# Performance work log

Measured on AMD Instinct MI355X. Metric: run time of the kernel, lower is better.

The kernel has to match this reference:

```python
import jax, jax.numpy as jnp
import numpy as np

BS, C, H, W, KSZ, NH = 4, 64, 64, 64, 7, 8
CH = 8 * C  # positional FFN hidden width (channels*8)


def _extract_nbhd(x, k):
    """x: (bs,h,w,d) -> (bs, h*w, k*k, d). Zero-padded k x k neighborhoods
    (the torch module unfolds the *projected* features, so padding zeros are
    zero keys/values, exactly as here)."""
    bs, h, w, d = x.shape
    p = k - 1
    xp = jnp.pad(x, ((0, 0), (p // 2, p - p // 2), (p // 2, p - p // 2), (0, 0)))
    shifts = [xp[:, di:di + h, dj:dj + w, :] for di in range(k) for dj in range(k)]
    patches = jnp.stack(shifts, axis=3)  # (bs, h, w, r, d)
    return patches.reshape(bs, h * w, k * k, d)


def setup_inputs() -> dict:
    key = jax.random.key(0)
    ks = jax.random.split(key, 8)

    def lin_w(kk, fan_in, fan_out):
        s = 1.0 / np.sqrt(fan_in)
        return jax.random.uniform(kk, (fan_in, fan_out), jnp.float32, -s, s)

    return {
        "x": jax.random.normal(ks[0], (BS, C, H, W), jnp.float32),
        "WQ_w": lin_w(ks[1], C, C), "WQ_b": jnp.zeros((C,), jnp.float32),
        "WK_w": lin_w(ks[2], C, C), "WK_b": jnp.zeros((C,), jnp.float32),
        "WV_w": lin_w(ks[3], C, C), "WV_b": jnp.zeros((C,), jnp.float32),
        "WO_w": lin_w(ks[4], C, C), "WO_b": jnp.zeros((C,), jnp.float32),
        "pos_w1": lin_w(ks[5], 2, CH), "pos_b1": jnp.zeros((CH,), jnp.float32),
        "pos_w2": lin_w(ks[6], CH, NH), "pos_b2": jnp.zeros((NH,), jnp.float32),
    }


def reference(x, WQ_w, WQ_b, WK_w, WK_b, WV_w, WV_b, WO_w, WO_b,
              pos_w1, pos_b1, pos_w2, pos_b2):
    bs, c, h, w = x.shape
    n, r, nh = h * w, KSZ * KSZ, NH
    dh = c // nh

    # ---- positional bias: FFN on relative coordinates of each k x k window ----
    gi, gj = jnp.meshgrid(jnp.linspace(-3.0, 3.0, h), jnp.linspace(-3.0, 3.0, w),
                          indexing='ij')
    coords = jnp.stack([gi, gj], axis=-1)                 # (h, w, 2)
    nb_coords = _extract_nbhd(coords[None], KSZ)          # (1, n, r, 2)
    rel = nb_coords - coords.reshape(1, n, 1, 2)          # (1, n, r, 2)
    P = jax.nn.relu(rel @ pos_w1 + pos_b1) @ pos_w2 + pos_b2   # (1, n, r, nh)

    # ---- restricted multi-head self attention over k x k neighborhoods ----
    xi = x.transpose(0, 2, 3, 1)                          # (bs, h, w, c)
    Q = (xi.reshape(bs, n, c) @ WQ_w + WQ_b).reshape(bs, n, nh, dh)
    Kn = _extract_nbhd(xi @ WK_w + WK_b, KSZ).reshape(bs, n, r, nh, dh)
    Vn = _extract_nbhd(xi @ WV_w + WV_b, KSZ).reshape(bs, n, r, nh, dh)

    scores = jnp.einsum('bnhd,bnrhd->bnhr', Q, Kn) / np.sqrt(dh).astype(np.float32)
    scores = scores + P.transpose(0, 1, 3, 2)             # bias per head, broadcast bs
    wts = jax.nn.softmax(scores, axis=-1)                 # (bs, n, nh, r)
    o = jnp.einsum('bnhr,bnrhd->bnhd', wts, Vn).reshape(bs, n, c)
    o = o @ WO_w + WO_b
    return o.reshape(bs, h, w, c).transpose(0, 3, 1, 2)   # (bs, c, h, w)
```

## Files before the change

kernel.cpp:

```cpp
#include <hip/hip_runtime.h>
#include <hip/hip_bf16.h>
#include <math.h>

#define NPIX   4096
#define STEPF  (6.0f/63.0f)
#define SCALE  0.35355339059327373f

#define OFF_PT 0
#define OFF_PB 4096
#define OFF_Q  65536
#define OFF_K  (OFF_Q + 1048576)
#define OFF_V  (OFF_K + 1048576)
#define OFF_O  (OFF_V + 1048576)

__global__ __launch_bounds__(256) void pos_ffn_kernel(
    const float* __restrict__ w1, const float* __restrict__ b1,
    const float* __restrict__ w2, const float* __restrict__ b2,
    float* __restrict__ PT, float* __restrict__ PB)
{
    __shared__ float s_w1[1024];
    __shared__ float s_b1[512];
    __shared__ float s_w2[4096];
    int tid = threadIdx.x;
    for (int idx = tid; idx < 5632; idx += 256) {
        if (idx < 1024)       s_w1[idx]        = w1[idx];
        else if (idx < 1536)  s_b1[idx - 1024] = b1[idx - 1024];
        else                  s_w2[idx - 1536] = w2[idx - 1536];
    }
    __syncthreads();

    int gid = blockIdx.x * 256 + tid;
    int e  = gid >> 3;
    int lg = gid & 7;
    if (e >= 49 + NPIX) return;

    float r0, r1;
    if (e < 49) {
        int di = e / 7, dj = e % 7;
        r0 = (float)(di - 3) * STEPF;
        r1 = (float)(dj - 3) * STEPF;
    } else {
        int p = e - 49;
        r0 = 3.0f - (float)(p >> 6) * STEPF;
        r1 = 3.0f - (float)(p & 63) * STEPF;
    }

    float acc[8] = {0.f,0.f,0.f,0.f,0.f,0.f,0.f,0.f};
    #pragma unroll 8
    for (int kk = 0; kk < 64; ++kk) {
        int k = (kk << 3) + lg;
        float hv = fmaf(r0, s_w1[k], fmaf(r1, s_w1[512 + k], s_b1[k]));
        hv = fmaxf(hv, 0.0f);
        const float4 wa = *(const float4*)&s_w2[k * 8];
        const float4 wb = *(const float4*)&s_w2[k * 8 + 4];
        acc[0] = fmaf(hv, wa.x, acc[0]);
        acc[1] = fmaf(hv, wa.y, acc[1]);
        acc[2] = fmaf(hv, wa.z, acc[2]);
        acc[3] = fmaf(hv, wa.w, acc[3]);
        acc[4] = fmaf(hv, wb.x, acc[4]);
        acc[5] = fmaf(hv, wb.y, acc[5]);
        acc[6] = fmaf(hv, wb.z, acc[6]);
        acc[7] = fmaf(hv, wb.w, acc[7]);
    }
    #pragma unroll
    for (int m = 1; m < 8; m <<= 1) {
        #pragma unroll
        for (int j = 0; j < 8; ++j) acc[j] += __shfl_xor(acc[j], m);
    }
    float v = acc[lg] + b2[lg];
    if (e < 49) PT[e * 8 + lg] = v;
    else        PB[(e - 49) * 8 + lg] = v;
}

__global__ __launch_bounds__(256) void qkv_kernel(
    const float* __restrict__ x,
    const float* __restrict__ wq, const float* __restrict__ bq,
    const float* __restrict__ wk, const float* __restrict__ bk,
    const float* __restrict__ wv, const float* __restrict__ bv,
    float* __restrict__ Qo, float* __restrict__ Ko, float* __restrict__ Vo)
{
    __shared__ float s_W[4096];
    __shared__ float s_b[64];
    const float* W; const float* bias; float* out;
    if (blockIdx.y == 0)      { W = wq; bias = bq; out = Qo; }
    else if (blockIdx.y == 1) { W = wk; bias = bk; out = Ko; }
    else                      { W = wv; bias = bv; out = Vo; }

    int tid = threadIdx.x;
    {
        const float4* W4 = (const float4*)W;
        float4* s4 = (float4*)s_W;
        #pragma unroll
        for (int q = 0; q < 4; ++q) s4[tid + q * 256] = W4[tid + q * 256];
    }
    if (tid < 64) s_b[tid] = bias[tid];
    __syncthreads();

    int jg = tid & 3;
    int pl = tid >> 2;
    int g  = blockIdx.x * 64 + pl;
    int b  = g >> 12;
    int p  = g & 4095;
    const float* xb = x + ((size_t)b << 18) + p;

    float acc[16];
    #pragma unroll
    for (int j = 0; j < 16; ++j) acc[j] = s_b[(jg << 4) + j];

    #pragma unroll 8
    for (int c = 0; c < 64; ++c) {
        float xv = xb[(size_t)c << 12];
        const float* wr = &s_W[(c << 6) + (jg << 4)];
        const float4 w0 = *(const float4*)(wr + 0);
        const float4 w1v = *(const float4*)(wr + 4);
        const float4 w2v = *(const float4*)(wr + 8);
        const float4 w3v = *(const float4*)(wr + 12);
        acc[0]  = fmaf(xv, w0.x,  acc[0]);  acc[1]  = fmaf(xv, w0.y,  acc[1]);
        acc[2]  = fmaf(xv, w0.z,  acc[2]);  acc[3]  = fmaf(xv, w0.w,  acc[3]);
        acc[4]  = fmaf(xv, w1v.x, acc[4]);  acc[5]  = fmaf(xv, w1v.y, acc[5]);
        acc[6]  = fmaf(xv, w1v.z, acc[6]);  acc[7]  = fmaf(xv, w1v.w, acc[7]);
        acc[8]  = fmaf(xv, w2v.x, acc[8]);  acc[9]  = fmaf(xv, w2v.y, acc[9]);
        acc[10] = fmaf(xv, w2v.z, acc[10]); acc[11] = fmaf(xv, w2v.w, acc[11]);
        acc[12] = fmaf(xv, w3v.x, acc[12]); acc[13] = fmaf(xv, w3v.y, acc[13]);
        acc[14] = fmaf(xv, w3v.z, acc[14]); acc[15] = fmaf(xv, w3v.w, acc[15]);
    }

    float* op = out + (size_t)g * 64 + (jg << 4);
    *(float4*)(op + 0)  = make_float4(acc[0],  acc[1],  acc[2],  acc[3]);
    *(float4*)(op + 4)  = make_float4(acc[4],  acc[5],  acc[6],  acc[7]);
    *(float4*)(op + 8)  = make_float4(acc[8],  acc[9],  acc[10], acc[11]);
    *(float4*)(op + 12) = make_float4(acc[12], acc[13], acc[14], acc[15]);
}

__global__ __launch_bounds__(256) void attn_kernel(
    const float* __restrict__ Q, const float* __restrict__ K,
    const float* __restrict__ V, const float* __restrict__ PT,
    const float* __restrict__ PB, float* __restrict__ O)
{
    __shared__ float s_PT[49 * 8];
    int tid = threadIdx.x;
    for (int idx = tid; idx < 49 * 8; idx += 256) s_PT[idx] = PT[idx];
    __syncthreads();

    int t = blockIdx.x * 256 + tid;
    int h = t & 7;
    int p = (t >> 3) & 4095;
    int b = t >> 15;
    int i = p >> 6, j = p & 63;

    const float* qp = Q + ((size_t)((b << 12) + p) << 6) + (h << 3);
    const float4 qa = *(const float4*)qp;
    const float4 qb = *(const float4*)(qp + 4);
    const float* Kbh = K + ((size_t)b << 18) + (h << 3);
    const float* Vbh = V + ((size_t)b << 18) + (h << 3);
    const float pb = PB[(p << 3) + h];

    float sc[49];
    float mx = -1e30f;
    #pragma unroll
    for (int di = 0; di < 7; ++di) {
        int i2 = i + di - 3;
        bool iok = (unsigned)i2 < 64u;
        int i2c = i2 < 0 ? 0 : (i2 > 63 ? 63 : i2);
        #pragma unroll
        for (int dj = 0; dj < 7; ++dj) {
            int j2 = j + dj - 3;
            bool ok = iok && ((unsigned)j2 < 64u);
            int j2c = j2 < 0 ? 0 : (j2 > 63 ? 63 : j2);
            const float* kp = Kbh + (i2c << 12) + (j2c << 6);
            const float4 ka = *(const float4*)kp;
            const float4 kb = *(const float4*)(kp + 4);
            float da = fmaf(qa.y, ka.y, qa.x * ka.x);
            da = fmaf(qa.w, ka.w, fmaf(qa.z, ka.z, da));
            float db = fmaf(qb.y, kb.y, qb.x * kb.x);
            db = fmaf(qb.w, kb.w, fmaf(qb.z, kb.z, db));
            int r = di * 7 + dj;
            float s = fmaf(da + db, SCALE, s_PT[(r << 3) + h]);
            s = ok ? s : pb;
            sc[r] = s;
            mx = fmaxf(mx, s);
        }
    }

    float sum = 0.0f;
    float o0=0.f,o1=0.f,o2=0.f,o3=0.f,o4=0.f,o5=0.f,o6=0.f,o7=0.f;
    #pragma unroll
    for (int di = 0; di < 7; ++di) {
        int i2 = i + di - 3;
        bool iok = (unsigned)i2 < 64u;
        int i2c = i2 < 0 ? 0 : (i2 > 63 ? 63 : i2);
        #pragma unroll
        for (int dj = 0; dj < 7; ++dj) {
            int j2 = j + dj - 3;
            bool ok = iok && ((unsigned)j2 < 64u);
            int j2c = j2 < 0 ? 0 : (j2 > 63 ? 63 : j2);
            int r = di * 7 + dj;
            float e = __expf(sc[r] - mx);
            sum += e;
            float ew = ok ? e : 0.0f;
            const float* vp = Vbh + (i2c << 12) + (j2c << 6);
            const float4 va = *(const float4*)vp;
            const float4 vb = *(const float4*)(vp + 4);
            o0 = fmaf(ew, va.x, o0); o1 = fmaf(ew, va.y, o1);
            o2 = fmaf(ew, va.z, o2); o3 = fmaf(ew, va.w, o3);
            o4 = fmaf(ew, vb.x, o4); o5 = fmaf(ew, vb.y, o5);
            o6 = fmaf(ew, vb.z, o6); o7 = fmaf(ew, vb.w, o7);
        }
    }
    float inv = 1.0f / sum;
    float* op = O + ((size_t)((b << 12) + p) << 6) + (h << 3);
    *(float4*)op       = make_float4(o0 * inv, o1 * inv, o2 * inv, o3 * inv);
    *(float4*)(op + 4) = make_float4(o4 * inv, o5 * inv, o6 * inv, o7 * inv);
}

__global__ __launch_bounds__(256) void outproj_kernel(
    const float* __restrict__ O, const float* __restrict__ W,
    const float* __restrict__ bias, float* __restrict__ out)
{
    __shared__ float s_W[4096];
    __shared__ float s_O[64 * 65];
    __shared__ float s_b[64];
    int tid = threadIdx.x;
    {
        const float4* W4 = (const float4*)W;
        float4* s4 = (float4*)s_W;
        #pragma unroll
        for (int q = 0; q < 4; ++q) s4[tid + q * 256] = W4[tid + q * 256];
    }
    if (tid < 64) s_b[tid] = bias[tid];

    int g0 = blockIdx.x * 64;
    const float4* O4 = (const float4*)(O + (size_t)g0 * 64);
    #pragma unroll
    for (int q = 0; q < 4; ++q) {
        int f4 = tid + q * 256;
        float4 v = O4[f4];
        int p_t = f4 >> 4;
        int c_t = (f4 & 15) << 2;
        float* d = &s_O[p_t * 65 + c_t];
        d[0] = v.x; d[1] = v.y; d[2] = v.z; d[3] = v.w;
    }
    __syncthreads();

    int pl = tid & 63;
    int cg = tid >> 6;
    float acc[16];
    #pragma unroll
    for (int j = 0; j < 16; ++j) acc[j] = s_b[(cg << 4) + j];

    #pragma unroll 8
    for (int c = 0; c < 64; ++c) {
        float xv = s_O[pl * 65 + c];
        const float* wr = &s_W[(c << 6) + (cg << 4)];
        const float4 w0 = *(const float4*)(wr + 0);
        const float4 w1v = *(const float4*)(wr + 4);
        const float4 w2v = *(const float4*)(wr + 8);
        const float4 w3v = *(const float4*)(wr + 12);
        acc[0]  = fmaf(xv, w0.x,  acc[0]);  acc[1]  = fmaf(xv, w0.y,  acc[1]);
        acc[2]  = fmaf(xv, w0.z,  acc[2]);  acc[3]  = fmaf(xv, w0.w,  acc[3]);
        acc[4]  = fmaf(xv, w1v.x, acc[4]);  acc[5]  = fmaf(xv, w1v.y, acc[5]);
        acc[6]  = fmaf(xv, w1v.z, acc[6]);  acc[7]  = fmaf(xv, w1v.w, acc[7]);
        acc[8]  = fmaf(xv, w2v.x, acc[8]);  acc[9]  = fmaf(xv, w2v.y, acc[9]);
        acc[10] = fmaf(xv, w2v.z, acc[10]); acc[11] = fmaf(xv, w2v.w, acc[11]);
        acc[12] = fmaf(xv, w3v.x, acc[12]); acc[13] = fmaf(xv, w3v.y, acc[13]);
        acc[14] = fmaf(xv, w3v.z, acc[14]); acc[15] = fmaf(xv, w3v.w, acc[15]);
    }

    int g = g0 + pl;
    int b = g >> 12, p = g & 4095;
    float* ob = out + ((size_t)b << 18) + p;
    #pragma unroll
    for (int j = 0; j < 16; ++j) ob[(size_t)((cg << 4) + j) << 12] = acc[j];
}

extern "C" void kernel_launch(void* const* d_in, const int* in_sizes, int n_in,
                              void* d_out, int out_size, void* d_ws, size_t ws_size,
                              hipStream_t stream) {
    const float* x    = (const float*)d_in[0];
    const float* WQw  = (const float*)d_in[1];
    const float* WQb  = (const float*)d_in[2];
    const float* WKw  = (const float*)d_in[3];
    const float* WKb  = (const float*)d_in[4];
    const float* WVw  = (const float*)d_in[5];
    const float* WVb  = (const float*)d_in[6];
    const float* WOw  = (const float*)d_in[7];
    const float* WOb  = (const float*)d_in[8];
    const float* pw1  = (const float*)d_in[9];
    const float* pb1  = (const float*)d_in[10];
    const float* pw2  = (const float*)d_in[11];
    const float* pb2  = (const float*)d_in[12];

    float* ws = (float*)d_ws;
    float* PT = ws + OFF_PT;
    float* PB = ws + OFF_PB;
    float* Qb = ws + OFF_Q;
    float* Kb = ws + OFF_K;
    float* Vb = ws + OFF_V;
    float* Ob = ws + OFF_O;

    pos_ffn_kernel<<<((49 + NPIX) * 8 + 255) / 256, 256, 0, stream>>>(
        pw1, pb1, pw2, pb2, PT, PB);
    qkv_kernel<<<dim3(16384 / 64, 3), 256, 0, stream>>>(
        x, WQw, WQb, WKw, WKb, WVw, WVb, Qb, Kb, Vb);
    attn_kernel<<<131072 / 256, 256, 0, stream>>>(Qb, Kb, Vb, PT, PB, Ob);
    outproj_kernel<<<16384 / 64, 256, 0, stream>>>(Ob, WOw, WOb, (float*)d_out);
}
```

Measured before the change: 56.68 us.

## Fuse output projection into attention kernel and double pixels per QKV thread

The output projection is folded into the attention kernel. Each block stages its 32 pixels' attention outputs in shared memory, then multiplies them by WO held in shared memory. This removes the O round trip through global memory and one kernel launch. The price is reloading the full 16KB WO into every one of 512 attention blocks and adding a barrier, which raises LDS use and may cut occupancy. Separately, the QKV kernel now computes two pixels per thread so each shared-memory weight load is reused twice, with half as many blocks.

```diff
diff --git a/kernel.cpp b/kernel.cpp
--- a/kernel.cpp
+++ b/kernel.cpp
@@ -11,7 +11,6 @@
 #define OFF_Q  65536
 #define OFF_K  (OFF_Q + 1048576)
 #define OFF_V  (OFF_K + 1048576)
-#define OFF_O  (OFF_V + 1048576)
 
 __global__ __launch_bounds__(256) void pos_ffn_kernel(
     const float* __restrict__ w1, const float* __restrict__ b1,
@@ -98,48 +97,76 @@
 
     int jg = tid & 3;
     int pl = tid >> 2;
-    int g  = blockIdx.x * 64 + pl;
-    int b  = g >> 12;
-    int p  = g & 4095;
-    const float* xb = x + ((size_t)b << 18) + p;
-
-    float acc[16];
-    #pragma unroll
-    for (int j = 0; j < 16; ++j) acc[j] = s_b[(jg << 4) + j];
-
-    #pragma unroll 8
+    int g0 = blockIdx.x * 128;
+    int b  = g0 >> 12;
+    int p0 = g0 & 4095;
+    const float* xb = x + ((size_t)b << 18) + p0 + pl;
+
+    float accA[16], accB[16];
+    #pragma unroll
+    for (int jj = 0; jj < 16; ++jj) {
+        float bv_ = s_b[(jg << 4) + jj];
+        accA[jj] = bv_; accB[jj] = bv_;
+    }
+
+    #pragma unroll 4
     for (int c = 0; c < 64; ++c) {
-        float xv = xb[(size_t)c << 12];
+        float xa = xb[(size_t)c << 12];
+        float xc = xb[((size_t)c << 12) + 64];
         const float* wr = &s_W[(c << 6) + (jg << 4)];
         const float4 w0 = *(const float4*)(wr + 0);
         const float4 w1v = *(const float4*)(wr + 4);
         const float4 w2v = *(const float4*)(wr + 8);
         const float4 w3v = *(const float4*)(wr + 12);
-        acc[0]  = fmaf(xv, w0.x,  acc[0]);  acc[1]  = fmaf(xv, w0.y,  acc[1]);
-        acc[2]  = fmaf(xv, w0.z,  acc[2]);  acc[3]  = fmaf(xv, w0.w,  acc[3]);
-        acc[4]  = fmaf(xv, w1v.x, acc[4]);  acc[5]  = fmaf(xv, w1v.y, acc[5]);
-        acc[6]  = fmaf(xv, w1v.z, acc[6]);  acc[7]  = fmaf(xv, w1v.w, acc[7]);
-        acc[8]  = fmaf(xv, w2v.x, acc[8]);  acc[9]  = fmaf(xv, w2v.y, acc[9]);
-        acc[10] = fmaf(xv, w2v.z, acc[10]); acc[11] = fmaf(xv, w2v.w, acc[11]);
-        acc[12] = fmaf(xv, w3v.x, acc[12]); acc[13] = fmaf(xv, w3v.y, acc[13]);
-        acc[14] = fmaf(xv, w3v.z, acc[14]); acc[15] = fmaf(xv, w3v.w, acc[15]);
-    }
-
-    float* op = out + (size_t)g * 64 + (jg << 4);
-    *(float4*)(op + 0)  = make_float4(acc[0],  acc[1],  acc[2],  acc[3]);
-    *(float4*)(op + 4)  = make_float4(acc[4],  acc[5],  acc[6],  acc[7]);
-    *(float4*)(op + 8)  = make_float4(acc[8],  acc[9],  acc[10], acc[11]);
-    *(float4*)(op + 12) = make_float4(acc[12], acc[13], acc[14], acc[15]);
+        accA[0]  = fmaf(xa, w0.x,  accA[0]);  accB[0]  = fmaf(xc, w0.x,  accB[0]);
+        accA[1]  = fmaf(xa, w0.y,  accA[1]);  accB[1]  = fmaf(xc, w0.y,  accB[1]);
+        accA[2]  = fmaf(xa, w0.z,  accA[2]);  accB[2]  = fmaf(xc, w0.z,  accB[2]);
+        accA[3]  = fmaf(xa, w0.w,  accA[3]);  accB[3]  = fmaf(xc, w0.w,  accB[3]);
+        accA[4]  = fmaf(xa, w1v.x, accA[4]);  accB[4]  = fmaf(xc, w1v.x, accB[4]);
+        accA[5]  = fmaf(xa, w1v.y, accA[5]);  accB[5]  = fmaf(xc, w1v.y, accB[5]);
+        accA[6]  = fmaf(xa, w1v.z, accA[6]);  accB[6]  = fmaf(xc, w1v.z, accB[6]);
+        accA[7]  = fmaf(xa, w1v.w, accA[7]);  accB[7]  = fmaf(xc, w1v.w, accB[7]);
+        accA[8]  = fmaf(xa, w2v.x, accA[8]);  accB[8]  = fmaf(xc, w2v.x, accB[8]);
+        accA[9]  = fmaf(xa, w2v.y, accA[9]);  accB[9]  = fmaf(xc, w2v.y, accB[9]);
+        accA[10] = fmaf(xa, w2v.z, accA[10]); accB[10] = fmaf(xc, w2v.z, accB[10]);
+        accA[11] = fmaf(xa, w2v.w, accA[11]); accB[11] = fmaf(xc, w2v.w, accB[11]);
+        accA[12] = fmaf(xa, w3v.x, accA[12]); accB[12] = fmaf(xc, w3v.x, accB[12]);
+        accA[13] = fmaf(xa, w3v.y, accA[13]); accB[13] = fmaf(xc, w3v.y, accB[13]);
+        accA[14] = fmaf(xa, w3v.z, accA[14]); accB[14] = fmaf(xc, w3v.z, accB[14]);
+        accA[15] = fmaf(xa, w3v.w, accA[15]); accB[15] = fmaf(xc, w3v.w, accB[15]);
+    }
+
+    float* opA = out + (size_t)(g0 + pl) * 64 + (jg << 4);
+    float* opB = opA + 64 * 64;
+    *(float4*)(opA + 0)  = make_float4(accA[0],  accA[1],  accA[2],  accA[3]);
+    *(float4*)(opA + 4)  = make_float4(accA[4],  accA[5],  accA[6],  accA[7]);
+    *(float4*)(opA + 8)  = make_float4(accA[8],  accA[9],  accA[10], accA[11]);
+    *(float4*)(opA + 12) = make_float4(accA[12], accA[13], accA[14], accA[15]);
+    *(float4*)(opB + 0)  = make_float4(accB[0],  accB[1],  accB[2],  accB[3]);
+    *(float4*)(opB + 4)  = make_float4(accB[4],  accB[5],  accB[6],  accB[7]);
+    *(float4*)(opB + 8)  = make_float4(accB[8],  accB[9],  accB[10], accB[11]);
+    *(float4*)(opB + 12) = make_float4(accB[12], accB[13], accB[14], accB[15]);
 }
 
-__global__ __launch_bounds__(256) void attn_kernel(
+__global__ __launch_bounds__(256) void attn_fused_kernel(
     const float* __restrict__ Q, const float* __restrict__ K,
     const float* __restrict__ V, const float* __restrict__ PT,
-    const float* __restrict__ PB, float* __restrict__ O)
+    const float* __restrict__ PB, const float* __restrict__ WO,
+    const float* __restrict__ bO, float* __restrict__ out)
 {
-    __shared__ float s_PT[49 * 8];
+    __shared__ float s_PT[392];
+    __shared__ float s_W[4096];
+    __shared__ float s_b[64];
+    __shared__ float s_O[32 * 68];
     int tid = threadIdx.x;
-    for (int idx = tid; idx < 49 * 8; idx += 256) s_PT[idx] = PT[idx];
+    {
+        const float4* W4 = (const float4*)WO;
+        float4* s4 = (float4*)s_W;
+        #pragma unroll
+        for (int q = 0; q < 4; ++q) s4[tid + q * 256] = W4[tid + q * 256];
+    }
+    for (int idx = tid; idx < 392; idx += 256) s_PT[idx] = PT[idx];
+    if (tid < 64) s_b[tid] = bO[tid];
     __syncthreads();
 
     int t = blockIdx.x * 256 + tid;
@@ -208,69 +235,38 @@
         }
     }
     float inv = 1.0f / sum;
-    float* op = O + ((size_t)((b << 12) + p) << 6) + (h << 3);
-    *(float4*)op       = make_float4(o0 * inv, o1 * inv, o2 * inv, o3 * inv);
-    *(float4*)(op + 4) = make_float4(o4 * inv, o5 * inv, o6 * inv, o7 * inv);
-}
-
-__global__ __launch_bounds__(256) void outproj_kernel(
-    const float* __restrict__ O, const float* __restrict__ W,
-    const float* __restrict__ bias, float* __restrict__ out)
-{
-    __shared__ float s_W[4096];
-    __shared__ float s_O[64 * 65];
-    __shared__ float s_b[64];
-    int tid = threadIdx.x;
     {
-        const float4* W4 = (const float4*)W;
-        float4* s4 = (float4*)s_W;
-        #pragma unroll
-        for (int q = 0; q < 4; ++q) s4[tid + q * 256] = W4[tid + q * 256];
-    }
-    if (tid < 64) s_b[tid] = bias[tid];
-
-    int g0 = blockIdx.x * 64;
-    const float4* O4 = (const float4*)(O + (size_t)g0 * 64);
-    #pragma unroll
-    for (int q = 0; q < 4; ++q) {
-        int f4 = tid + q * 256;
-        float4 v = O4[f4];
-        int p_t = f4 >> 4;
-        int c_t = (f4 & 15) << 2;
-        float* d = &s_O[p_t * 65 + c_t];
-        d[0] = v.x; d[1] = v.y; d[2] = v.z; d[3] = v.w;
+        int pl = (tid >> 3) & 31;
+        float* so = &s_O[pl * 68 + (h << 3)];
+        *(float4*)(so + 0) = make_float4(o0 * inv, o1 * inv, o2 * inv, o3 * inv);
+        *(float4*)(so + 4) = make_float4(o4 * inv, o5 * inv, o6 * inv, o7 * inv);
     }
     __syncthreads();
 
-    int pl = tid & 63;
-    int cg = tid >> 6;
-    float acc[16];
-    #pragma unroll
-    for (int j = 0; j < 16; ++j) acc[j] = s_b[(cg << 4) + j];
+    int pl2 = tid & 31;
+    int cg  = tid >> 5;
+    float acc[8];
+    #pragma unroll
+    for (int k = 0; k < 8; ++k) acc[k] = s_b[(cg << 3) + k];
 
     #pragma unroll 8
     for (int c = 0; c < 64; ++c) {
-        float xv = s_O[pl * 65 + c];
-        const float* wr = &s_W[(c << 6) + (cg << 4)];
-        const float4 w0 = *(const float4*)(wr + 0);
-        const float4 w1v = *(const float4*)(wr + 4);
-        const float4 w2v = *(const float4*)(wr + 8);
-        const float4 w3v = *(const float4*)(wr + 12);
-        acc[0]  = fmaf(xv, w0.x,  acc[0]);  acc[1]  = fmaf(xv, w0.y,  acc[1]);
-        acc[2]  = fmaf(xv, w0.z,  acc[2]);  acc[3]  = fmaf(xv, w0.w,  acc[3]);
-        acc[4]  = fmaf(xv, w1v.x, acc[4]);  acc[5]  = fmaf(xv, w1v.y, acc[5]);
-        acc[6]  = fmaf(xv, w1v.z, acc[6]);  acc[7]  = fmaf(xv, w1v.w, acc[7]);
-        acc[8]  = fmaf(xv, w2v.x, acc[8]);  acc[9]  = fmaf(xv, w2v.y, acc[9]);
-        acc[10] = fmaf(xv, w2v.z, acc[10]); acc[11] = fmaf(xv, w2v.w, acc[11]);
-        acc[12] = fmaf(xv, w3v.x, acc[12]); acc[13] = fmaf(xv, w3v.y, acc[13]);
-        acc[14] = fmaf(xv, w3v.z, acc[14]); acc[15] = fmaf(xv, w3v.w, acc[15]);
-    }
-
-    int g = g0 + pl;
-    int b = g >> 12, p = g & 4095;
-    float* ob = out + ((size_t)b << 18) + p;
-    #pragma unroll
-    for (int j = 0; j < 16; ++j) ob[(size_t)((cg << 4) + j) << 12] = acc[j];
+        float xv = s_O[pl2 * 68 + c];
+        const float* wr = &s_W[(c << 6) + (cg << 3)];
+        const float4 wa = *(const float4*)wr;
+        const float4 wb = *(const float4*)(wr + 4);
+        acc[0] = fmaf(xv, wa.x, acc[0]); acc[1] = fmaf(xv, wa.y, acc[1]);
+        acc[2] = fmaf(xv, wa.z, acc[2]); acc[3] = fmaf(xv, wa.w, acc[3]);
+        acc[4] = fmaf(xv, wb.x, acc[4]); acc[5] = fmaf(xv, wb.y, acc[5]);
+        acc[6] = fmaf(xv, wb.z, acc[6]); acc[7] = fmaf(xv, wb.w, acc[7]);
+    }
+
+    int g0 = blockIdx.x * 32;
+    int bb = g0 >> 12;
+    int pp = (g0 & 4095) + pl2;
+    float* ob = out + ((size_t)bb << 18) + pp;
+    #pragma unroll
+    for (int k = 0; k < 8; ++k) ob[(size_t)((cg << 3) + k) << 12] = acc[k];
 }
 
 extern "C" void kernel_launch(void* const* d_in, const int* in_sizes, int n_in,
@@ -296,12 +292,11 @@
     float* Qb = ws + OFF_Q;
     float* Kb = ws + OFF_K;
     float* Vb = ws + OFF_V;
-    float* Ob = ws + OFF_O;
 
     pos_ffn_kernel<<<((49 + NPIX) * 8 + 255) / 256, 256, 0, stream>>>(
         pw1, pb1, pw2, pb2, PT, PB);
-    qkv_kernel<<<dim3(16384 / 64, 3), 256, 0, stream>>>(
+    qkv_kernel<<<dim3(16384 / 128, 3), 256, 0, stream>>>(
         x, WQw, WQb, WKw, WKb, WVw, WVb, Qb, Kb, Vb);
-    attn_kernel<<<131072 / 256, 256, 0, stream>>>(Qb, Kb, Vb, PT, PB, Ob);
-    outproj_kernel<<<16384 / 64, 256, 0, stream>>>(Ob, WOw, WOb, (float*)d_out);
+    attn_fused_kernel<<<131072 / 256, 256, 0, stream>>>(
+        Qb, Kb, Vb, PT, PB, WOw, WOb, (float*)d_out);
 }
```

Result: faster. 55.21 us (-2.6%).
